# Kernel tuning notes

Measured on AMD Instinct MI355X. Metric: run time of the kernel, lower is better.

## Reference

```python
import jax, jax.numpy as jnp
import numpy as np

B, S_DEC, S_ENC, D, H = 2, 2048, 2048, 1024, 16
HD = D // H  # 64


def setup_inputs() -> dict:
    key = jax.random.key(0)
    ks = jax.random.split(key, 12)
    s = 0.02
    return {
        "dec_hidden_state": jax.random.normal(ks[0], (B, S_DEC, D), jnp.float32),
        "enc_hidden_state": jax.random.normal(ks[1], (B, S_ENC, D), jnp.float32),
        "mask": jnp.ones((B, S_ENC, S_DEC), jnp.int32),
        "Wq": jax.random.normal(ks[2], (H, D, HD), jnp.float32) * s,
        "bq": jax.random.normal(ks[3], (H, HD), jnp.float32) * s,
        "Wk": jax.random.normal(ks[4], (H, D, HD), jnp.float32) * s,
        "bk": jax.random.normal(ks[5], (H, HD), jnp.float32) * s,
        "Wv": jax.random.normal(ks[6], (H, D, HD), jnp.float32) * s,
        "bv": jax.random.normal(ks[7], (H, HD), jnp.float32) * s,
        "Wo": jax.random.normal(ks[8], (D, D), jnp.float32) * s,
        "bo": jax.random.normal(ks[9], (D,), jnp.float32) * s,
    }


def reference(dec_hidden_state, enc_hidden_state, mask, Wq, bq, Wk, bk, Wv, bv, Wo, bo):
    # NOTE: original module swaps args: query <- enc_hidden_state, key/value <- dec_hidden_state.
    # q: [B,H,S_enc,HD], k/v: [B,H,S_dec,HD]
    q = jnp.einsum("bqd,hdk->bhqk", enc_hidden_state, Wq) + bq[None, :, None, :]
    k = jnp.einsum("bsd,hdk->bhsk", dec_hidden_state, Wk) + bk[None, :, None, :]
    v = jnp.einsum("bsd,hdk->bhsk", dec_hidden_state, Wv) + bv[None, :, None, :]
    scores = jnp.einsum("bhqk,bhsk->bhqs", q, k) / jnp.sqrt(jnp.asarray(HD, q.dtype))
    scores = jnp.where(mask[:, None, :, :] == 0, jnp.asarray(-jnp.inf, scores.dtype), scores)
    weights = jax.nn.softmax(scores, axis=-1)
    attn = jnp.einsum("bhqs,bhsk->bhqk", weights, v)  # [B,H,S_enc,HD]
    # concat heads along last dim (same order as torch.cat over head list)
    attn = jnp.transpose(attn, (0, 2, 1, 3)).reshape(B, S_ENC, D)
    return attn @ Wo + bo
```

## Files before the change

kernel.cpp:

```cpp
#include <hip/hip_runtime.h>
#include <math.h>
#include <stdint.h>


typedef unsigned short ushort_t;
typedef __attribute__((ext_vector_type(8))) short short8;
typedef __attribute__((ext_vector_type(4))) float floatx4;

__device__ __forceinline__ ushort_t f2bf(float x){
  unsigned u = __float_as_uint(x);
  u += 0x7fffu + ((u >> 16) & 1u);
  return (ushort_t)(u >> 16);
}
__device__ __forceinline__ unsigned pk2bf(float a, float b){
#if __has_builtin(__builtin_amdgcn_cvt_pk_bf16_f32)
  typedef __attribute__((ext_vector_type(2))) __bf16 bf2_t;
  bf2_t r = __builtin_amdgcn_cvt_pk_bf16_f32(a, b);
  return *(unsigned*)&r;
#else
  return (unsigned)f2bf(a) | ((unsigned)f2bf(b) << 16);
#endif
}
__device__ __forceinline__ floatx4 mfma16(short8 a, short8 b, floatx4 c){
  return __builtin_amdgcn_mfma_f32_16x16x32_bf16(a, b, c, 0, 0, 0);
}
__device__ __forceinline__ void async_copy16(const void* g, void* l){
  __builtin_amdgcn_global_load_lds((const __attribute__((address_space(1))) void*)g,
                                   (__attribute__((address_space(3))) void*)l,
                                   16, 0, 0);
}

__global__ void conv_bf16_kernel(const float* __restrict__ s0, const float* __restrict__ s1,
                                 ushort_t* __restrict__ d0, ushort_t* __restrict__ d1){
  const float* src = blockIdx.y ? s1 : s0;
  ushort_t*    dst = blockIdx.y ? d1 : d0;
  int i = (blockIdx.x * 256 + threadIdx.x) * 4;
  const float4 v = *(const float4*)(src + i);
  unsigned long long p = (unsigned long long)f2bf(v.x)
                       | ((unsigned long long)f2bf(v.y) << 16)
                       | ((unsigned long long)f2bf(v.z) << 32)
                       | ((unsigned long long)f2bf(v.w) << 48);
  *(unsigned long long*)(dst + i) = p;
}

__global__ void transpose_pack_kernel(const float* __restrict__ src, ushort_t* __restrict__ dst,
                                      int R, int C, long srcHead, long dstHead){
  __shared__ float t[64][65];
  const int tid = threadIdx.x;
  const long sb = (long)blockIdx.z * srcHead;
  const long db = (long)blockIdx.z * dstHead;
  const int r0 = blockIdx.y * 64, c0 = blockIdx.x * 64;
  #pragma unroll
  for (int i = 0; i < 16; i++){
    int idx = i*256 + tid;
    int r = idx >> 6, c = idx & 63;
    t[r][c] = src[sb + (long)(r0 + r)*C + c0 + c];
  }
  __syncthreads();
  #pragma unroll
  for (int i = 0; i < 16; i++){
    int idx = i*256 + tid;
    int cr = idx >> 6, rc = idx & 63;
    dst[db + (long)(c0 + cr)*R + r0 + rc] = f2bf(t[rc][cr]);
  }
}

__global__ void transpose_pack_qkv_kernel(const float* __restrict__ Wq, const float* __restrict__ Wk,
                                          const float* __restrict__ Wv,
                                          ushort_t* __restrict__ WqT, ushort_t* __restrict__ WkT,
                                          ushort_t* __restrict__ WvT){
  __shared__ float t[64][65];
  const int tid = threadIdx.x;
  const int which = blockIdx.z >> 4, head = blockIdx.z & 15;
  const float* src = (which == 0) ? Wq : (which == 1) ? Wk : Wv;
  ushort_t*    dst = (which == 0) ? WqT : (which == 1) ? WkT : WvT;
  const long sb = (long)head * 65536;
  const long db = (long)head * 65536;
  const int r0 = blockIdx.y * 64;
  #pragma unroll
  for (int i = 0; i < 16; i++){
    int idx = i*256 + tid;
    int r = idx >> 6, c = idx & 63;
    t[r][c] = src[sb + (long)(r0 + r)*64 + c];
  }
  __syncthreads();
  #pragma unroll
  for (int i = 0; i < 16; i++){
    int idx = i*256 + tid;
    int cr = idx >> 6, rc = idx & 63;
    dst[db + (long)cr*1024 + r0 + rc] = f2bf(t[rc][cr]);
  }
}

__global__ void maskpack_kernel(const int* __restrict__ mask, unsigned long long* __restrict__ mb){
  long gid = (long)blockIdx.x * 256 + threadIdx.x;
  unsigned long long bal = __ballot(mask[gid] != 0);
  if ((threadIdx.x & 63) == 0) mb[gid >> 6] = bal;
}

__global__ __launch_bounds__(256, 3)
void gemm_qkv_kernel(const ushort_t* __restrict__ encb, const ushort_t* __restrict__ decb,
                     const ushort_t* __restrict__ WqT, const ushort_t* __restrict__ WkT,
                     const ushort_t* __restrict__ WvT,
                     const float* __restrict__ bq, const float* __restrict__ bk,
                     const float* __restrict__ bv,
                     ushort_t* __restrict__ Qb, ushort_t* __restrict__ Kbf,
                     ushort_t* __restrict__ Vtb)
{
  __shared__ ushort_t At[128*32];
  __shared__ ushort_t Bt[128*32];
  const int tid = threadIdx.x;
  const int wave = tid >> 6, lane = tid & 63;
  const int quad = lane >> 4, l16 = lane & 15;
  const int z = blockIdx.z;
  const ushort_t *A, *BT; const float* bias; ushort_t* outp;
  int m0, n0; long outAdj = 0;
  if (z == 0){ A = encb; BT = WqT; bias = bq; outp = Qb;  m0 = blockIdx.y*128; n0 = blockIdx.x*128; }
  else if (z == 1){ A = decb; BT = WkT; bias = bk; outp = Kbf; m0 = blockIdx.y*128; n0 = blockIdx.x*128; }
  else {
    int id = blockIdx.y*8 + blockIdx.x;
    int vb = id >> 7, rem = id & 127;
    m0 = ((rem >> 4) & 7) * 128; n0 = (rem & 15) * 128;
    A = WvT; BT = decb + (long)vb*2097152; bias = bv; outp = Vtb; outAdj = (long)vb*2097152;
  }
  const int K = 1024;

  const int c0 = tid, c1 = 256 + tid;
  const ushort_t* gA0 = A  + (long)(m0 + (c0 >> 2))*K + (c0 & 3)*8;
  const ushort_t* gA1 = A  + (long)(m0 + (c1 >> 2))*K + (c1 & 3)*8;
  const ushort_t* gB0 = BT + (long)(n0 + (c0 >> 2))*K + (c0 & 3)*8;
  const ushort_t* gB1 = BT + (long)(n0 + (c1 >> 2))*K + (c1 & 3)*8;
  ushort_t* lA0 = &At[wave*512];
  ushort_t* lA1 = &At[(4+wave)*512];
  ushort_t* lB0 = &Bt[wave*512];
  ushort_t* lB1 = &Bt[(4+wave)*512];

  floatx4 acc[4][4];
  #pragma unroll
  for (int mt = 0; mt < 4; mt++)
    #pragma unroll
    for (int nt = 0; nt < 4; nt++)
      acc[mt][nt] = (floatx4){0.f, 0.f, 0.f, 0.f};

  const int moff = (wave & 1) * 64, noff = (wave >> 1) * 64;
  for (int k0 = 0; k0 < K; k0 += 32){
    __syncthreads();
    async_copy16(gA0, lA0);
    async_copy16(gA1, lA1);
    async_copy16(gB0, lB0);
    async_copy16(gB1, lB1);
    gA0 += 32; gA1 += 32; gB0 += 32; gB1 += 32;
    __syncthreads();
    short8 af[4], bfr[4];
    #pragma unroll
    for (int t = 0; t < 4; t++){
      af[t]  = *(const short8*)&At[(moff + t*16 + l16)*32 + quad*8];
      bfr[t] = *(const short8*)&Bt[(noff + t*16 + l16)*32 + quad*8];
    }
    #pragma unroll
    for (int mt = 0; mt < 4; mt++)
      #pragma unroll
      for (int nt = 0; nt < 4; nt++)
        acc[mt][nt] = mfma16(af[mt], bfr[nt], acc[mt][nt]);
  }

  #pragma unroll
  for (int mt = 0; mt < 4; mt++){
    #pragma unroll
    for (int nt = 0; nt < 4; nt++){
      const int col = n0 + noff + nt*16 + l16;
      const int rowb = m0 + moff + mt*16 + quad*4;
      #pragma unroll
      for (int reg = 0; reg < 4; reg++){
        const int row = rowb + reg;
        float v = acc[mt][nt][reg];
        if (z < 2){
          v += bias[col];
          long o = ((long)(row >> 11)*16 + (col >> 6))*131072
                 + (long)(row & 2047)*64 + (col & 63);
          outp[o] = f2bf(v);
        } else {
          v += bias[row];
          outp[outAdj + (long)row*2048 + col] = f2bf(v);
        }
      }
    }
  }
}

__global__ __launch_bounds__(256, 2)
void gemm_o_kernel(const ushort_t* __restrict__ A, const ushort_t* __restrict__ BT,
                   const float* __restrict__ bias, float* __restrict__ outf)
{
  __shared__ ushort_t At[128*32];
  __shared__ ushort_t Bt[64*32];
  const int tid = threadIdx.x;
  const int wave = tid >> 6, lane = tid & 63;
  const int quad = lane >> 4, l16 = lane & 15;
  const int m0 = blockIdx.y * 128, n0 = blockIdx.x * 64;
  const int K = 1024;

  const int c0 = tid, c1 = 256 + tid;
  const ushort_t* gA0 = A  + (long)(m0 + (c0 >> 2))*K + (c0 & 3)*8;
  const ushort_t* gA1 = A  + (long)(m0 + (c1 >> 2))*K + (c1 & 3)*8;
  const ushort_t* gB0 = BT + (long)(n0 + (c0 >> 2))*K + (c0 & 3)*8;
  ushort_t* lA0 = &At[wave*512];
  ushort_t* lA1 = &At[(4+wave)*512];
  ushort_t* lB0 = &Bt[wave*512];

  floatx4 acc[4][2];
  #pragma unroll
  for (int mt = 0; mt < 4; mt++)
    #pragma unroll
    for (int nt = 0; nt < 2; nt++)
      acc[mt][nt] = (floatx4){0.f, 0.f, 0.f, 0.f};

  const int moff = (wave & 1) * 64, noff = (wave >> 1) * 32;
  for (int k0 = 0; k0 < K; k0 += 32){
    __syncthreads();
    async_copy16(gA0, lA0);
    async_copy16(gA1, lA1);
    async_copy16(gB0, lB0);
    gA0 += 32; gA1 += 32; gB0 += 32;
    __syncthreads();
    short8 af[4], bfr[2];
    #pragma unroll
    for (int t = 0; t < 4; t++)
      af[t]  = *(const short8*)&At[(moff + t*16 + l16)*32 + quad*8];
    #pragma unroll
    for (int t = 0; t < 2; t++)
      bfr[t] = *(const short8*)&Bt[(noff + t*16 + l16)*32 + quad*8];
    #pragma unroll
    for (int mt = 0; mt < 4; mt++)
      #pragma unroll
      for (int nt = 0; nt < 2; nt++)
        acc[mt][nt] = mfma16(af[mt], bfr[nt], acc[mt][nt]);
  }

  #pragma unroll
  for (int mt = 0; mt < 4; mt++){
    #pragma unroll
    for (int nt = 0; nt < 2; nt++){
      const int col = n0 + noff + nt*16 + l16;
      const int rowb = m0 + moff + mt*16 + quad*4;
      #pragma unroll
      for (int reg = 0; reg < 4; reg++)
        outf[(long)(rowb + reg)*1024 + col] = acc[mt][nt][reg] + bias[col];
    }
  }
}

__global__ __launch_bounds__(512, 4)
void flash_attn_kernel(const ushort_t* __restrict__ Q, const ushort_t* __restrict__ Kb,
                       const ushort_t* __restrict__ Vt, const unsigned* __restrict__ mb,
                       ushort_t* __restrict__ aout)
{
  __shared__ ushort_t KV[18432];
  __shared__ ushort_t Psm[18432];
  ushort_t* Kt0 = KV;
  ushort_t* Kt1 = KV + 4608;
  ushort_t* Vt0 = KV + 9216;
  ushort_t* Vt1 = KV + 13824;

  const int tid = threadIdx.x, wave = tid >> 6, lane = tid & 63;
  const int wq = wave & 3, par = wave >> 2;
  const int quad = lane >> 4, l16 = lane & 15;
  const int bh = blockIdx.x, qt = blockIdx.y;
  const int b = bh >> 4, h = bh & 15;
  const float C = 0.18033688011112042f;

  const ushort_t* KB = Kb + (long)bh*131072;
  const ushort_t* VB = Vt + (long)bh*131072;
  const int q0 = qt*128 + wq*32;

  short8 qf[2][2];
  #pragma unroll
  for (int mtq = 0; mtq < 2; mtq++)
    #pragma unroll
    for (int ks = 0; ks < 2; ks++)
      qf[mtq][ks] = *(const short8*)&Q[((long)bh*2048 + q0 + mtq*16 + l16)*64 + ks*32 + quad*8];

  floatx4 accO[2][4];
  #pragma unroll
  for (int mtq = 0; mtq < 2; mtq++)
    #pragma unroll
    for (int ht = 0; ht < 4; ht++) accO[mtq][ht] = (floatx4){0.f,0.f,0.f,0.f};
  float lsum[2] = {0.f, 0.f};

  const int srow = tid >> 3, scol = (tid & 7) * 8;
  const ushort_t* gKp = KB + srow*64 + scol;
  const ushort_t* gVp = VB + (long)srow*2048 + scol;
  ushort_t* lK = &Kt0[srow*72 + scol];
  ushort_t* lV = &Vt0[srow*72 + scol];
  ushort_t* Pp = &Psm[wave*2304];

  const ushort_t* Kp = par ? Kt1 : Kt0;
  const ushort_t* Vp = par ? Vt1 : Vt0;
  const uint2* mb2 = (const uint2*)mb;
  const long mbase = ((long)b*2048 + q0);

  short8 gk0 = *(const short8*)(gKp);
  short8 gk1 = *(const short8*)(gKp + 4096);
  short8 gv0 = *(const short8*)(gVp);
  short8 gv1 = *(const short8*)(gVp + 64);
  gKp += 8192; gVp += 128;

  for (int r = 0; r < 16; r++){
    *(short8*)(lK)        = gk0;
    *(short8*)(lK + 4608) = gk1;
    *(short8*)(lV)        = gv0;
    *(short8*)(lV + 4608) = gv1;
    __syncthreads();
    if (r < 15){
      gk0 = *(const short8*)(gKp);
      gk1 = *(const short8*)(gKp + 4096);
      gv0 = *(const short8*)(gVp);
      gv1 = *(const short8*)(gVp + 64);
      gKp += 8192; gVp += 128;
    }
    const int st = 2*r + par;

    uint2 mw[2];
    #pragma unroll
    for (int mtq = 0; mtq < 2; mtq++)
      mw[mtq] = mb2[(mbase + mtq*16 + l16)*32 + st];
    const bool uni = __all((mw[0].x & mw[0].y & mw[1].x & mw[1].y) == 0xFFFFFFFFu);

    #pragma unroll
    for (int mtile = 0; mtile < 4; mtile++){
      short8 kf0 = *(const short8*)&Kp[(mtile*16 + l16)*72 + quad*8];
      short8 kf1 = *(const short8*)&Kp[(mtile*16 + l16)*72 + 32 + quad*8];
      #pragma unroll
      for (int mtq = 0; mtq < 2; mtq++){
        floatx4 zz = (floatx4){0.f,0.f,0.f,0.f};
        zz = mfma16(kf0, qf[mtq][0], zz);
        zz = mfma16(kf1, qf[mtq][1], zz);
        float p0 = __builtin_amdgcn_exp2f(zz[0]*C);
        float p1 = __builtin_amdgcn_exp2f(zz[1]*C);
        float p2 = __builtin_amdgcn_exp2f(zz[2]*C);
        float p3 = __builtin_amdgcn_exp2f(zz[3]*C);
        if (__builtin_expect(!uni, 0)){
          const unsigned w = (&mw[mtq].x)[mtile >> 1];
          const int sh = (mtile & 1)*16 + quad*4;
          p0 = ((w >> (sh+0)) & 1u) ? p0 : 0.f;
          p1 = ((w >> (sh+1)) & 1u) ? p1 : 0.f;
          p2 = ((w >> (sh+2)) & 1u) ? p2 : 0.f;
          p3 = ((w >> (sh+3)) & 1u) ? p3 : 0.f;
        }
        lsum[mtq] += (p0 + p1) + (p2 + p3);
        uint2 pk; pk.x = pk2bf(p0, p1); pk.y = pk2bf(p2, p3);
        *(uint2*)&Pp[(mtq*16 + l16)*72 + mtile*16 + quad*4] = pk;
      }
    }
    #pragma unroll
    for (int ks = 0; ks < 2; ks++){
      short8 pf0 = *(const short8*)&Pp[(l16)*72 + ks*32 + quad*8];
      short8 pf1 = *(const short8*)&Pp[(16 + l16)*72 + ks*32 + quad*8];
      #pragma unroll
      for (int ht = 0; ht < 4; ht++){
        short8 vf = *(const short8*)&Vp[(ht*16 + l16)*72 + ks*32 + quad*8];
        accO[0][ht] = mfma16(pf0, vf, accO[0][ht]);
        accO[1][ht] = mfma16(pf1, vf, accO[1][ht]);
      }
    }
    __syncthreads();
  }

  #pragma unroll
  for (int mtq = 0; mtq < 2; mtq++){
    lsum[mtq] += __shfl_xor(lsum[mtq], 16);
    lsum[mtq] += __shfl_xor(lsum[mtq], 32);
  }

  float* Of = (float*)KV;
  float* Ls = ((float*)KV) + 128*68;
  if (par == 1){
    #pragma unroll
    for (int mtq = 0; mtq < 2; mtq++){
      #pragma unroll
      for (int ht = 0; ht < 4; ht++)
        #pragma unroll
        for (int reg = 0; reg < 4; reg++)
          Of[(wq*32 + mtq*16 + quad*4 + reg)*68 + ht*16 + l16] = accO[mtq][ht][reg];
      if (quad == 0) Ls[wq*32 + mtq*16 + l16] = lsum[mtq];
    }
  }
  __syncthreads();
  if (par == 0){
    #pragma unroll
    for (int mtq = 0; mtq < 2; mtq++){
      const float tot = lsum[mtq] + Ls[wq*32 + mtq*16 + l16];
      #pragma unroll
      for (int reg = 0; reg < 4; reg++){
        const float inv = 1.0f / __shfl(tot, quad*4 + reg);
        const int q = q0 + mtq*16 + quad*4 + reg;
        const long rowo = ((long)b*2048 + q)*1024 + h*64;
        #pragma unroll
        for (int ht = 0; ht < 4; ht++){
          float v = accO[mtq][ht][reg] + Of[(wq*32 + mtq*16 + quad*4 + reg)*68 + ht*16 + l16];
          aout[rowo + ht*16 + l16] = f2bf(v * inv);
        }
      }
    }
  }
}

extern "C" void kernel_launch(void* const* d_in, const int* in_sizes, int n_in,
                              void* d_out, int out_size, void* d_ws, size_t ws_size,
                              hipStream_t stream) {
  const float* dec  = (const float*)d_in[0];
  const float* enc  = (const float*)d_in[1];
  const int*   mask = (const int*)d_in[2];
  const float* Wq   = (const float*)d_in[3];
  const float* bq   = (const float*)d_in[4];
  const float* Wk   = (const float*)d_in[5];
  const float* bk   = (const float*)d_in[6];
  const float* Wv   = (const float*)d_in[7];
  const float* bv   = (const float*)d_in[8];
  const float* Wo   = (const float*)d_in[9];
  const float* bo   = (const float*)d_in[10];
  float* out = (float*)d_out;

  ushort_t* ws   = (ushort_t*)d_ws;
  ushort_t* encb = ws;
  ushort_t* decb = encb + 4194304;
  ushort_t* Qb   = decb + 4194304;
  ushort_t* Kbf  = Qb   + 4194304;
  ushort_t* Vtb  = Kbf  + 4194304;
  ushort_t* WqT  = Vtb  + 4194304;
  ushort_t* WkT  = WqT  + 1048576;
  ushort_t* WvT  = WkT  + 1048576;
  ushort_t* WoT  = WvT  + 1048576;
  unsigned* Mb   = (unsigned*)(WoT + 1048576);

  conv_bf16_kernel<<<dim3(4096,2,1), 256, 0, stream>>>(enc, dec, encb, decb);
  transpose_pack_qkv_kernel<<<dim3(1,16,48), 256, 0, stream>>>(Wq, Wk, Wv, WqT, WkT, WvT);
  transpose_pack_kernel<<<dim3(16,16,1), 256, 0, stream>>>(Wo, WoT, 1024, 1024, 0, 0);
  maskpack_kernel<<<32768, 256, 0, stream>>>(mask, (unsigned long long*)Mb);

  gemm_qkv_kernel<<<dim3(8,32,3), 256, 0, stream>>>(encb, decb, WqT, WkT, WvT,
                                                    bq, bk, bv, Qb, Kbf, Vtb);
  flash_attn_kernel<<<dim3(32,16,1), 512, 0, stream>>>(Qb, Kbf, Vtb, Mb, encb);
  gemm_o_kernel<<<dim3(16,32,1), 256, 0, stream>>>(encb, WoT, bo, out);
}
```

Baseline: 276.9 us.

## Fuse prep kernels, double-buffer GEMM tiles, restructure attention to keep P in registers

The four preprocessing launches (bf16 conversion, weight transposes, mask packing) become one prep kernel dispatched by block index, cutting launch overhead. Both GEMMs get double-buffered LDS tiles so the next K-slice's async copy overlaps the current MFMAs, and one barrier per step is dropped. The attention kernel drops the two-wave-group split over key tiles and the shared-memory merge. Each wave now owns 16 query rows and walks all 32 key tiles, feeding P straight from registers into a 16x16x16 MFMA for P·V. This avoids the P round-trip through LDS and the final reduction, at the cost of fewer query rows per wave and a smaller MFMA shape.

```diff
diff --git a/kernel.cpp b/kernel.cpp
--- a/kernel.cpp
+++ b/kernel.cpp
@@ -5,6 +5,7 @@
 
 typedef unsigned short ushort_t;
 typedef __attribute__((ext_vector_type(8))) short short8;
+typedef __attribute__((ext_vector_type(4))) short short4v;
 typedef __attribute__((ext_vector_type(4))) float floatx4;
 
 __device__ __forceinline__ ushort_t f2bf(float x){
@@ -24,78 +25,87 @@
 __device__ __forceinline__ floatx4 mfma16(short8 a, short8 b, floatx4 c){
   return __builtin_amdgcn_mfma_f32_16x16x32_bf16(a, b, c, 0, 0, 0);
 }
+#if __has_builtin(__builtin_amdgcn_mfma_f32_16x16x16bf16_1k)
+__device__ __forceinline__ floatx4 mfma_pv(short4v a, short4v b, floatx4 c){
+  return __builtin_amdgcn_mfma_f32_16x16x16bf16_1k(a, b, c, 0, 0, 0);
+}
+#else
+__device__ __forceinline__ floatx4 mfma_pv(short4v a, short4v b, floatx4 c){
+  short8 a8 = {a[0], a[1], a[2], a[3], 0, 0, 0, 0};
+  short8 b8 = {b[0], b[1], b[2], b[3], 0, 0, 0, 0};
+  return mfma16(a8, b8, c);
+}
+#endif
 __device__ __forceinline__ void async_copy16(const void* g, void* l){
   __builtin_amdgcn_global_load_lds((const __attribute__((address_space(1))) void*)g,
                                    (__attribute__((address_space(3))) void*)l,
                                    16, 0, 0);
 }
 
-__global__ void conv_bf16_kernel(const float* __restrict__ s0, const float* __restrict__ s1,
-                                 ushort_t* __restrict__ d0, ushort_t* __restrict__ d1){
-  const float* src = blockIdx.y ? s1 : s0;
-  ushort_t*    dst = blockIdx.y ? d1 : d0;
-  int i = (blockIdx.x * 256 + threadIdx.x) * 4;
-  const float4 v = *(const float4*)(src + i);
-  unsigned long long p = (unsigned long long)f2bf(v.x)
-                       | ((unsigned long long)f2bf(v.y) << 16)
-                       | ((unsigned long long)f2bf(v.z) << 32)
-                       | ((unsigned long long)f2bf(v.w) << 48);
-  *(unsigned long long*)(dst + i) = p;
-}
-
-__global__ void transpose_pack_kernel(const float* __restrict__ src, ushort_t* __restrict__ dst,
-                                      int R, int C, long srcHead, long dstHead){
+__global__ __launch_bounds__(256)
+void prep_kernel(const float* __restrict__ enc, const float* __restrict__ dec,
+                 const float* __restrict__ Wq, const float* __restrict__ Wk,
+                 const float* __restrict__ Wv, const float* __restrict__ Wo,
+                 const int* __restrict__ mask,
+                 ushort_t* __restrict__ encb, ushort_t* __restrict__ decb,
+                 ushort_t* __restrict__ WqT, ushort_t* __restrict__ WkT,
+                 ushort_t* __restrict__ WvT, ushort_t* __restrict__ WoT,
+                 unsigned long long* __restrict__ mb)
+{
   __shared__ float t[64][65];
-  const int tid = threadIdx.x;
-  const long sb = (long)blockIdx.z * srcHead;
-  const long db = (long)blockIdx.z * dstHead;
-  const int r0 = blockIdx.y * 64, c0 = blockIdx.x * 64;
-  #pragma unroll
-  for (int i = 0; i < 16; i++){
-    int idx = i*256 + tid;
-    int r = idx >> 6, c = idx & 63;
-    t[r][c] = src[sb + (long)(r0 + r)*C + c0 + c];
-  }
-  __syncthreads();
-  #pragma unroll
-  for (int i = 0; i < 16; i++){
-    int idx = i*256 + tid;
-    int cr = idx >> 6, rc = idx & 63;
-    dst[db + (long)(c0 + cr)*R + r0 + rc] = f2bf(t[rc][cr]);
-  }
-}
-
-__global__ void transpose_pack_qkv_kernel(const float* __restrict__ Wq, const float* __restrict__ Wk,
-                                          const float* __restrict__ Wv,
-                                          ushort_t* __restrict__ WqT, ushort_t* __restrict__ WkT,
-                                          ushort_t* __restrict__ WvT){
-  __shared__ float t[64][65];
-  const int tid = threadIdx.x;
-  const int which = blockIdx.z >> 4, head = blockIdx.z & 15;
-  const float* src = (which == 0) ? Wq : (which == 1) ? Wk : Wv;
-  ushort_t*    dst = (which == 0) ? WqT : (which == 1) ? WkT : WvT;
-  const long sb = (long)head * 65536;
-  const long db = (long)head * 65536;
-  const int r0 = blockIdx.y * 64;
-  #pragma unroll
-  for (int i = 0; i < 16; i++){
-    int idx = i*256 + tid;
-    int r = idx >> 6, c = idx & 63;
-    t[r][c] = src[sb + (long)(r0 + r)*64 + c];
-  }
-  __syncthreads();
-  #pragma unroll
-  for (int i = 0; i < 16; i++){
-    int idx = i*256 + tid;
-    int cr = idx >> 6, rc = idx & 63;
-    dst[db + (long)cr*1024 + r0 + rc] = f2bf(t[rc][cr]);
-  }
-}
-
-__global__ void maskpack_kernel(const int* __restrict__ mask, unsigned long long* __restrict__ mb){
-  long gid = (long)blockIdx.x * 256 + threadIdx.x;
-  unsigned long long bal = __ballot(mask[gid] != 0);
-  if ((threadIdx.x & 63) == 0) mb[gid >> 6] = bal;
+  const int bx = blockIdx.x, tid = threadIdx.x;
+  if (bx < 8192){
+    const float* src = (bx < 4096) ? enc : dec;
+    ushort_t*    dst = (bx < 4096) ? encb : decb;
+    int i = ((bx & 4095) * 256 + tid) * 4;
+    const float4 v = *(const float4*)(src + i);
+    unsigned long long p = (unsigned long long)f2bf(v.x)
+                         | ((unsigned long long)f2bf(v.y) << 16)
+                         | ((unsigned long long)f2bf(v.z) << 32)
+                         | ((unsigned long long)f2bf(v.w) << 48);
+    *(unsigned long long*)(dst + i) = p;
+  } else if (bx < 8960){
+    const int id = bx - 8192;
+    const int zz = id >> 4, yy = id & 15;
+    const int which = zz >> 4, head = zz & 15;
+    const float* src = (which == 0) ? Wq : (which == 1) ? Wk : Wv;
+    ushort_t*    dst = (which == 0) ? WqT : (which == 1) ? WkT : WvT;
+    const long sb = (long)head * 65536;
+    const int r0 = yy * 64;
+    #pragma unroll
+    for (int i = 0; i < 16; i++){
+      int idx = i*256 + tid;
+      int r = idx >> 6, c = idx & 63;
+      t[r][c] = src[sb + (long)(r0 + r)*64 + c];
+    }
+    __syncthreads();
+    #pragma unroll
+    for (int i = 0; i < 16; i++){
+      int idx = i*256 + tid;
+      int cr = idx >> 6, rc = idx & 63;
+      dst[sb + (long)cr*1024 + r0 + rc] = f2bf(t[rc][cr]);
+    }
+  } else if (bx < 9216){
+    const int id = bx - 8960;
+    const int r0 = (id >> 4) * 64, c0 = (id & 15) * 64;
+    #pragma unroll
+    for (int i = 0; i < 16; i++){
+      int idx = i*256 + tid;
+      int r = idx >> 6, c = idx & 63;
+      t[r][c] = Wo[(long)(r0 + r)*1024 + c0 + c];
+    }
+    __syncthreads();
+    #pragma unroll
+    for (int i = 0; i < 16; i++){
+      int idx = i*256 + tid;
+      int cr = idx >> 6, rc = idx & 63;
+      WoT[(long)(c0 + cr)*1024 + r0 + rc] = f2bf(t[rc][cr]);
+    }
+  } else {
+    long gid = (long)(bx - 9216) * 256 + tid;
+    unsigned long long bal = __ballot(mask[gid] != 0);
+    if ((tid & 63) == 0) mb[gid >> 6] = bal;
+  }
 }
 
 __global__ __launch_bounds__(256, 3)
@@ -107,8 +117,8 @@
                      ushort_t* __restrict__ Qb, ushort_t* __restrict__ Kbf,
                      ushort_t* __restrict__ Vtb)
 {
-  __shared__ ushort_t At[128*32];
-  __shared__ ushort_t Bt[128*32];
+  __shared__ ushort_t At[2*4096];
+  __shared__ ushort_t Bt[2*4096];
   const int tid = threadIdx.x;
   const int wave = tid >> 6, lane = tid & 63;
   const int quad = lane >> 4, l16 = lane & 15;
@@ -130,10 +140,6 @@
   const ushort_t* gA1 = A  + (long)(m0 + (c1 >> 2))*K + (c1 & 3)*8;
   const ushort_t* gB0 = BT + (long)(n0 + (c0 >> 2))*K + (c0 & 3)*8;
   const ushort_t* gB1 = BT + (long)(n0 + (c1 >> 2))*K + (c1 & 3)*8;
-  ushort_t* lA0 = &At[wave*512];
-  ushort_t* lA1 = &At[(4+wave)*512];
-  ushort_t* lB0 = &Bt[wave*512];
-  ushort_t* lB1 = &Bt[(4+wave)*512];
 
   floatx4 acc[4][4];
   #pragma unroll
@@ -142,26 +148,36 @@
     for (int nt = 0; nt < 4; nt++)
       acc[mt][nt] = (floatx4){0.f, 0.f, 0.f, 0.f};
 
+  async_copy16(gA0, &At[wave*512]);
+  async_copy16(gA1, &At[(4+wave)*512]);
+  async_copy16(gB0, &Bt[wave*512]);
+  async_copy16(gB1, &Bt[(4+wave)*512]);
+  gA0 += 32; gA1 += 32; gB0 += 32; gB1 += 32;
+
   const int moff = (wave & 1) * 64, noff = (wave >> 1) * 64;
+  int cur = 0;
   for (int k0 = 0; k0 < K; k0 += 32){
     __syncthreads();
-    async_copy16(gA0, lA0);
-    async_copy16(gA1, lA1);
-    async_copy16(gB0, lB0);
-    async_copy16(gB1, lB1);
-    gA0 += 32; gA1 += 32; gB0 += 32; gB1 += 32;
-    __syncthreads();
+    if (k0 + 32 < K){
+      const int nx = cur ^ 1;
+      async_copy16(gA0, &At[nx*4096 + wave*512]);
+      async_copy16(gA1, &At[nx*4096 + (4+wave)*512]);
+      async_copy16(gB0, &Bt[nx*4096 + wave*512]);
+      async_copy16(gB1, &Bt[nx*4096 + (4+wave)*512]);
+      gA0 += 32; gA1 += 32; gB0 += 32; gB1 += 32;
+    }
     short8 af[4], bfr[4];
     #pragma unroll
     for (int t = 0; t < 4; t++){
-      af[t]  = *(const short8*)&At[(moff + t*16 + l16)*32 + quad*8];
-      bfr[t] = *(const short8*)&Bt[(noff + t*16 + l16)*32 + quad*8];
+      af[t]  = *(const short8*)&At[cur*4096 + (moff + t*16 + l16)*32 + quad*8];
+      bfr[t] = *(const short8*)&Bt[cur*4096 + (noff + t*16 + l16)*32 + quad*8];
     }
     #pragma unroll
     for (int mt = 0; mt < 4; mt++)
       #pragma unroll
       for (int nt = 0; nt < 4; nt++)
         acc[mt][nt] = mfma16(af[mt], bfr[nt], acc[mt][nt]);
+    cur ^= 1;
   }
 
   #pragma unroll
@@ -192,8 +208,8 @@
 void gemm_o_kernel(const ushort_t* __restrict__ A, const ushort_t* __restrict__ BT,
                    const float* __restrict__ bias, float* __restrict__ outf)
 {
-  __shared__ ushort_t At[128*32];
-  __shared__ ushort_t Bt[64*32];
+  __shared__ ushort_t At[2*4096];
+  __shared__ ushort_t Bt[2*2048];
   const int tid = threadIdx.x;
   const int wave = tid >> 6, lane = tid & 63;
   const int quad = lane >> 4, l16 = lane & 15;
@@ -204,9 +220,6 @@
   const ushort_t* gA0 = A  + (long)(m0 + (c0 >> 2))*K + (c0 & 3)*8;
   const ushort_t* gA1 = A  + (long)(m0 + (c1 >> 2))*K + (c1 & 3)*8;
   const ushort_t* gB0 = BT + (long)(n0 + (c0 >> 2))*K + (c0 & 3)*8;
-  ushort_t* lA0 = &At[wave*512];
-  ushort_t* lA1 = &At[(4+wave)*512];
-  ushort_t* lB0 = &Bt[wave*512];
 
   floatx4 acc[4][2];
   #pragma unroll
@@ -215,26 +228,35 @@
     for (int nt = 0; nt < 2; nt++)
       acc[mt][nt] = (floatx4){0.f, 0.f, 0.f, 0.f};
 
+  async_copy16(gA0, &At[wave*512]);
+  async_copy16(gA1, &At[(4+wave)*512]);
+  async_copy16(gB0, &Bt[wave*512]);
+  gA0 += 32; gA1 += 32; gB0 += 32;
+
   const int moff = (wave & 1) * 64, noff = (wave >> 1) * 32;
+  int cur = 0;
   for (int k0 = 0; k0 < K; k0 += 32){
     __syncthreads();
-    async_copy16(gA0, lA0);
-    async_copy16(gA1, lA1);
-    async_copy16(gB0, lB0);
-    gA0 += 32; gA1 += 32; gB0 += 32;
-    __syncthreads();
+    if (k0 + 32 < K){
+      const int nx = cur ^ 1;
+      async_copy16(gA0, &At[nx*4096 + wave*512]);
+      async_copy16(gA1, &At[nx*4096 + (4+wave)*512]);
+      async_copy16(gB0, &Bt[nx*2048 + wave*512]);
+      gA0 += 32; gA1 += 32; gB0 += 32;
+    }
     short8 af[4], bfr[2];
     #pragma unroll
     for (int t = 0; t < 4; t++)
-      af[t]  = *(const short8*)&At[(moff + t*16 + l16)*32 + quad*8];
+      af[t]  = *(const short8*)&At[cur*4096 + (moff + t*16 + l16)*32 + quad*8];
     #pragma unroll
     for (int t = 0; t < 2; t++)
-      bfr[t] = *(const short8*)&Bt[(noff + t*16 + l16)*32 + quad*8];
+      bfr[t] = *(const short8*)&Bt[cur*2048 + (noff + t*16 + l16)*32 + quad*8];
     #pragma unroll
     for (int mt = 0; mt < 4; mt++)
       #pragma unroll
       for (int nt = 0; nt < 2; nt++)
         acc[mt][nt] = mfma16(af[mt], bfr[nt], acc[mt][nt]);
+    cur ^= 1;
   }
 
   #pragma unroll
@@ -255,15 +277,9 @@
                        const ushort_t* __restrict__ Vt, const unsigned* __restrict__ mb,
                        ushort_t* __restrict__ aout)
 {
-  __shared__ ushort_t KV[18432];
-  __shared__ ushort_t Psm[18432];
-  ushort_t* Kt0 = KV;
-  ushort_t* Kt1 = KV + 4608;
-  ushort_t* Vt0 = KV + 9216;
-  ushort_t* Vt1 = KV + 13824;
-
+  __shared__ ushort_t Kbuf[2*4608];
+  __shared__ ushort_t Vbuf[2*4608];
   const int tid = threadIdx.x, wave = tid >> 6, lane = tid & 63;
-  const int wq = wave & 3, par = wave >> 2;
   const int quad = lane >> 4, l16 = lane & 15;
   const int bh = blockIdx.x, qt = blockIdx.y;
   const int b = bh >> 4, h = bh & 15;
@@ -271,137 +287,84 @@
 
   const ushort_t* KB = Kb + (long)bh*131072;
   const ushort_t* VB = Vt + (long)bh*131072;
-  const int q0 = qt*128 + wq*32;
-
-  short8 qf[2][2];
-  #pragma unroll
-  for (int mtq = 0; mtq < 2; mtq++)
-    #pragma unroll
-    for (int ks = 0; ks < 2; ks++)
-      qf[mtq][ks] = *(const short8*)&Q[((long)bh*2048 + q0 + mtq*16 + l16)*64 + ks*32 + quad*8];
-
-  floatx4 accO[2][4];
-  #pragma unroll
-  for (int mtq = 0; mtq < 2; mtq++)
-    #pragma unroll
-    for (int ht = 0; ht < 4; ht++) accO[mtq][ht] = (floatx4){0.f,0.f,0.f,0.f};
-  float lsum[2] = {0.f, 0.f};
+  const int q0 = qt*128 + wave*16;
+
+  short8 qf0 = *(const short8*)&Q[((long)bh*2048 + q0 + l16)*64 +      quad*8];
+  short8 qf1 = *(const short8*)&Q[((long)bh*2048 + q0 + l16)*64 + 32 + quad*8];
+
+  floatx4 accO[4];
+  #pragma unroll
+  for (int ht = 0; ht < 4; ht++) accO[ht] = (floatx4){0.f,0.f,0.f,0.f};
+  float lsum = 0.f;
 
   const int srow = tid >> 3, scol = (tid & 7) * 8;
   const ushort_t* gKp = KB + srow*64 + scol;
   const ushort_t* gVp = VB + (long)srow*2048 + scol;
-  ushort_t* lK = &Kt0[srow*72 + scol];
-  ushort_t* lV = &Vt0[srow*72 + scol];
-  ushort_t* Pp = &Psm[wave*2304];
-
-  const ushort_t* Kp = par ? Kt1 : Kt0;
-  const ushort_t* Vp = par ? Vt1 : Vt0;
+  const int loff = srow*72 + scol;
+
   const uint2* mb2 = (const uint2*)mb;
-  const long mbase = ((long)b*2048 + q0);
-
-  short8 gk0 = *(const short8*)(gKp);
-  short8 gk1 = *(const short8*)(gKp + 4096);
-  short8 gv0 = *(const short8*)(gVp);
-  short8 gv1 = *(const short8*)(gVp + 64);
-  gKp += 8192; gVp += 128;
-
-  for (int r = 0; r < 16; r++){
-    *(short8*)(lK)        = gk0;
-    *(short8*)(lK + 4608) = gk1;
-    *(short8*)(lV)        = gv0;
-    *(short8*)(lV + 4608) = gv1;
+  const long mbase = (long)b*2048 + q0;
+
+  short8 gk = *(const short8*)gKp;  gKp += 4096;
+  short8 gv = *(const short8*)gVp;  gVp += 64;
+
+  int cur = 0;
+  for (int st = 0; st < 32; st++){
+    *(short8*)&Kbuf[cur*4608 + loff] = gk;
+    *(short8*)&Vbuf[cur*4608 + loff] = gv;
     __syncthreads();
-    if (r < 15){
-      gk0 = *(const short8*)(gKp);
-      gk1 = *(const short8*)(gKp + 4096);
-      gv0 = *(const short8*)(gVp);
-      gv1 = *(const short8*)(gVp + 64);
-      gKp += 8192; gVp += 128;
-    }
-    const int st = 2*r + par;
-
-    uint2 mw[2];
-    #pragma unroll
-    for (int mtq = 0; mtq < 2; mtq++)
-      mw[mtq] = mb2[(mbase + mtq*16 + l16)*32 + st];
-    const bool uni = __all((mw[0].x & mw[0].y & mw[1].x & mw[1].y) == 0xFFFFFFFFu);
+    if (st < 31){
+      gk = *(const short8*)gKp;  gKp += 4096;
+      gv = *(const short8*)gVp;  gVp += 64;
+    }
+    const ushort_t* Kp = &Kbuf[cur*4608];
+    const ushort_t* Vp = &Vbuf[cur*4608];
+
+    uint2 mw = mb2[(mbase + l16)*32 + st];
+    const bool uni = __all((mw.x & mw.y) == 0xFFFFFFFFu);
 
     #pragma unroll
     for (int mtile = 0; mtile < 4; mtile++){
-      short8 kf0 = *(const short8*)&Kp[(mtile*16 + l16)*72 + quad*8];
+      short8 kf0 = *(const short8*)&Kp[(mtile*16 + l16)*72 +      quad*8];
       short8 kf1 = *(const short8*)&Kp[(mtile*16 + l16)*72 + 32 + quad*8];
-      #pragma unroll
-      for (int mtq = 0; mtq < 2; mtq++){
-        floatx4 zz = (floatx4){0.f,0.f,0.f,0.f};
-        zz = mfma16(kf0, qf[mtq][0], zz);
-        zz = mfma16(kf1, qf[mtq][1], zz);
-        float p0 = __builtin_amdgcn_exp2f(zz[0]*C);
-        float p1 = __builtin_amdgcn_exp2f(zz[1]*C);
-        float p2 = __builtin_amdgcn_exp2f(zz[2]*C);
-        float p3 = __builtin_amdgcn_exp2f(zz[3]*C);
-        if (__builtin_expect(!uni, 0)){
-          const unsigned w = (&mw[mtq].x)[mtile >> 1];
-          const int sh = (mtile & 1)*16 + quad*4;
-          p0 = ((w >> (sh+0)) & 1u) ? p0 : 0.f;
-          p1 = ((w >> (sh+1)) & 1u) ? p1 : 0.f;
-          p2 = ((w >> (sh+2)) & 1u) ? p2 : 0.f;
-          p3 = ((w >> (sh+3)) & 1u) ? p3 : 0.f;
-        }
-        lsum[mtq] += (p0 + p1) + (p2 + p3);
-        uint2 pk; pk.x = pk2bf(p0, p1); pk.y = pk2bf(p2, p3);
-        *(uint2*)&Pp[(mtq*16 + l16)*72 + mtile*16 + quad*4] = pk;
+      floatx4 zz = (floatx4){0.f,0.f,0.f,0.f};
+      zz = mfma16(kf0, qf0, zz);
+      zz = mfma16(kf1, qf1, zz);
+      float p0 = __builtin_amdgcn_exp2f(zz[0]*C);
+      float p1 = __builtin_amdgcn_exp2f(zz[1]*C);
+      float p2 = __builtin_amdgcn_exp2f(zz[2]*C);
+      float p3 = __builtin_amdgcn_exp2f(zz[3]*C);
+      if (__builtin_expect(!uni, 0)){
+        const unsigned w = (mtile & 2) ? mw.y : mw.x;
+        const int sh = (mtile & 1)*16 + quad*4;
+        p0 = ((w >> (sh+0)) & 1u) ? p0 : 0.f;
+        p1 = ((w >> (sh+1)) & 1u) ? p1 : 0.f;
+        p2 = ((w >> (sh+2)) & 1u) ? p2 : 0.f;
+        p3 = ((w >> (sh+3)) & 1u) ? p3 : 0.f;
       }
-    }
-    #pragma unroll
-    for (int ks = 0; ks < 2; ks++){
-      short8 pf0 = *(const short8*)&Pp[(l16)*72 + ks*32 + quad*8];
-      short8 pf1 = *(const short8*)&Pp[(16 + l16)*72 + ks*32 + quad*8];
+      lsum += (p0 + p1) + (p2 + p3);
+      uint2 pk; pk.x = pk2bf(p0, p1); pk.y = pk2bf(p2, p3);
+      const short4v pb = *(const short4v*)&pk;
       #pragma unroll
       for (int ht = 0; ht < 4; ht++){
-        short8 vf = *(const short8*)&Vp[(ht*16 + l16)*72 + ks*32 + quad*8];
-        accO[0][ht] = mfma16(pf0, vf, accO[0][ht]);
-        accO[1][ht] = mfma16(pf1, vf, accO[1][ht]);
+        short4v vf = *(const short4v*)&Vp[(ht*16 + l16)*72 + mtile*16 + quad*4];
+        accO[ht] = mfma_pv(vf, pb, accO[ht]);
       }
     }
-    __syncthreads();
-  }
-
-  #pragma unroll
-  for (int mtq = 0; mtq < 2; mtq++){
-    lsum[mtq] += __shfl_xor(lsum[mtq], 16);
-    lsum[mtq] += __shfl_xor(lsum[mtq], 32);
-  }
-
-  float* Of = (float*)KV;
-  float* Ls = ((float*)KV) + 128*68;
-  if (par == 1){
-    #pragma unroll
-    for (int mtq = 0; mtq < 2; mtq++){
-      #pragma unroll
-      for (int ht = 0; ht < 4; ht++)
-        #pragma unroll
-        for (int reg = 0; reg < 4; reg++)
-          Of[(wq*32 + mtq*16 + quad*4 + reg)*68 + ht*16 + l16] = accO[mtq][ht][reg];
-      if (quad == 0) Ls[wq*32 + mtq*16 + l16] = lsum[mtq];
-    }
-  }
-  __syncthreads();
-  if (par == 0){
-    #pragma unroll
-    for (int mtq = 0; mtq < 2; mtq++){
-      const float tot = lsum[mtq] + Ls[wq*32 + mtq*16 + l16];
-      #pragma unroll
-      for (int reg = 0; reg < 4; reg++){
-        const float inv = 1.0f / __shfl(tot, quad*4 + reg);
-        const int q = q0 + mtq*16 + quad*4 + reg;
-        const long rowo = ((long)b*2048 + q)*1024 + h*64;
-        #pragma unroll
-        for (int ht = 0; ht < 4; ht++){
-          float v = accO[mtq][ht][reg] + Of[(wq*32 + mtq*16 + quad*4 + reg)*68 + ht*16 + l16];
-          aout[rowo + ht*16 + l16] = f2bf(v * inv);
-        }
-      }
-    }
+    cur ^= 1;
+  }
+
+  lsum += __shfl_xor(lsum, 16);
+  lsum += __shfl_xor(lsum, 32);
+  const float inv = 1.0f / lsum;
+
+  const long rowo = ((long)b*2048 + q0 + l16)*1024 + h*64;
+  #pragma unroll
+  for (int ht = 0; ht < 4; ht++){
+    uint2 pk;
+    pk.x = pk2bf(accO[ht][0]*inv, accO[ht][1]*inv);
+    pk.y = pk2bf(accO[ht][2]*inv, accO[ht][3]*inv);
+    *(unsigned long long*)&aout[rowo + ht*16 + quad*4] = *(unsigned long long*)&pk;
   }
 }
 
@@ -433,11 +396,9 @@
   ushort_t* WoT  = WvT  + 1048576;
   unsigned* Mb   = (unsigned*)(WoT + 1048576);
 
-  conv_bf16_kernel<<<dim3(4096,2,1), 256, 0, stream>>>(enc, dec, encb, decb);
-  transpose_pack_qkv_kernel<<<dim3(1,16,48), 256, 0, stream>>>(Wq, Wk, Wv, WqT, WkT, WvT);
-  transpose_pack_kernel<<<dim3(16,16,1), 256, 0, stream>>>(Wo, WoT, 1024, 1024, 0, 0);
-  maskpack_kernel<<<32768, 256, 0, stream>>>(mask, (unsigned long long*)Mb);
-
+  prep_kernel<<<41984, 256, 0, stream>>>(enc, dec, Wq, Wk, Wv, Wo, mask,
+                                         encb, decb, WqT, WkT, WvT, WoT,
+                                         (unsigned long long*)Mb);
   gemm_qkv_kernel<<<dim3(8,32,3), 256, 0, stream>>>(encb, decb, WqT, WkT, WvT,
                                                     bq, bk, bv, Qb, Kbf, Vtb);
   flash_attn_kernel<<<dim3(32,16,1), 512, 0, stream>>>(Qb, Kbf, Vtb, Mb, encb);
```

Result: faster. 261.7 us (-5.5%).
